# Kernel optimization log

Measured on AMD Instinct MI355X. Metric: run time of the kernel, lower is better.

## Reference

```python
import jax, jax.numpy as jnp
import numpy as np
import math

# ---- static config (must match init_kwargs / input_specs) ----
D = 1024
N_HEAD = 16
HEAD_DIM = D // N_HEAD          # 64
HALF = HEAD_DIM // 2            # rope half dim = 32
N_EXP = 8
TOP_K = 2
CAP_FACTOR = 2.0
LN_EPS = 1e-5


def _build_sin_cos(T, half_dim, dtype=jnp.float32):
    pos = jnp.arange(T, dtype=dtype)[:, None]                      # (T,1)
    inv_freq = 1.0 / (10000.0 ** (jnp.arange(0, 2 * half_dim, 2, dtype=dtype) / (2 * half_dim)))
    ang = pos * inv_freq[None, :]                                  # (T, half)
    return jnp.sin(ang), jnp.cos(ang)


def _layernorm(x, g, b):
    mu = jnp.mean(x, axis=-1, keepdims=True)
    var = jnp.mean(jnp.square(x - mu), axis=-1, keepdims=True)
    return (x - mu) * jax.lax.rsqrt(var + LN_EPS) * g + b


def _apply_rope(q, k, sin, cos):
    # q,k: (B,T,H,hd); sin,cos: (T, half)
    s = sin[None, :, None, :]
    c = cos[None, :, None, :]
    q1, q2 = q[..., :HALF], q[..., HALF:]
    k1, k2 = k[..., :HALF], k[..., HALF:]
    qr = jnp.concatenate([q1 * c - q2 * s, q1 * s + q2 * c], axis=-1)
    kr = jnp.concatenate([k1 * c - k2 * s, k1 * s + k2 * c], axis=-1)
    return qr, kr


def _attention(x, Wqkv, Wproj):
    B, T, C = x.shape
    qkv = x @ Wqkv                                                  # (B,T,3C)
    qkv = qkv.reshape(B, T, N_HEAD, 3 * HEAD_DIM)
    q, k, v = jnp.split(qkv, 3, axis=-1)                            # each (B,T,H,hd)
    sin, cos = _build_sin_cos(T, HALF)
    q, k = _apply_rope(q, k, sin, cos)
    scale = 1.0 / math.sqrt(HEAD_DIM)
    att = jnp.einsum('bqhd,bkhd->bhqk', q, k) * scale               # (B,H,T,T)
    causal = jnp.tril(jnp.ones((T, T), dtype=bool))
    att = jnp.where(causal[None, None], att, jnp.finfo(att.dtype).min)
    p = jax.nn.softmax(att, axis=-1)
    o = jnp.einsum('bhqk,bkhd->bqhd', p, v).reshape(B, T, C)
    return o @ Wproj, k, v


def _sparse_moe(flat, Wgate, W1, b1, W2, b2):
    # flat: (N, d). Eval mode: no router noise.
    N, d = flat.shape
    capacity = int(math.ceil(CAP_FACTOR * N / N_EXP))
    logits = flat @ Wgate                                           # (N,E)
    gates = jax.nn.softmax(logits, axis=-1)
    vals, inds = jax.lax.top_k(gates, TOP_K)                        # (N,k)
    flat_inds = inds.reshape(-1)                                    # (N*k,)
    flat_vals = vals.reshape(-1)
    neg = jnp.finfo(flat.dtype).min
    # per-expert assignment scores over all (token, slot) pairs
    scores = jnp.where(flat_inds[None, :] == jnp.arange(N_EXP)[:, None],
                       flat_vals[None, :], neg)                     # (E, N*k)
    top_scores, top_pos = jax.lax.top_k(scores, capacity)           # (E, cap)
    tok_idx = top_pos // TOP_K                                      # (E, cap)
    w = jnp.where(top_scores > neg, top_scores, 0.0)                # dropped slots -> 0 weight
    xe = flat[tok_idx]                                              # gather: (E, cap, d)
    h = jax.nn.gelu(jnp.einsum('ecd,edh->ech', xe, W1) + b1[:, None, :], approximate=False)
    out = jnp.einsum('ech,ehd->ecd', h, W2) + b2[:, None, :]
    out = out * w[..., None]
    final = jnp.zeros_like(flat).at[tok_idx.reshape(-1)].add(out.reshape(-1, d))
    return final


def setup_inputs() -> dict:
    key = jax.random.key(0)
    ks = jax.random.split(key, 10)
    B, T = 2, 2048
    s = 0.02
    return {
        'x': jax.random.normal(ks[0], (B, T, D), dtype=jnp.float32),
        'ln1_g': jnp.ones((D,), jnp.float32),
        'ln1_b': jnp.zeros((D,), jnp.float32),
        'ln2_g': jnp.ones((D,), jnp.float32),
        'ln2_b': jnp.zeros((D,), jnp.float32),
        'Wqkv': jax.random.normal(ks[1], (D, 3 * D), jnp.float32) * s,
        'Wproj': jax.random.normal(ks[2], (D, D), jnp.float32) * s,
        'Wgate': jax.random.normal(ks[3], (D, N_EXP), jnp.float32) * s,
        'W1': jax.random.normal(ks[4], (N_EXP, D, 4 * D), jnp.float32) * s,
        'b1': jnp.zeros((N_EXP, 4 * D), jnp.float32),
        'W2': jax.random.normal(ks[5], (N_EXP, 4 * D, D), jnp.float32) * s,
        'b2': jnp.zeros((N_EXP, D), jnp.float32),
    }


def reference(x, ln1_g, ln1_b, ln2_g, ln2_b, Wqkv, Wproj, Wgate, W1, b1, W2, b2):
    B, T, _ = x.shape
    x_norm = _layernorm(x, ln1_g, ln1_b)
    attn_out, k, v = _attention(x_norm, Wqkv, Wproj)
    x = x + attn_out
    ff_in = _layernorm(x, ln2_g, ln2_b)
    moe_out = _sparse_moe(ff_in.reshape(B * T, D), Wgate, W1, b1, W2, b2)
    x = x + moe_out.reshape(B, T, D)
    aux_loss = jnp.zeros((), x.dtype)  # eval mode
    return x, aux_loss, k, v
```

## Files before the change

### kernel.cpp

```cpp
#include <hip/hip_runtime.h>
#include <hip/hip_bf16.h>
#include <math.h>


#define TT 2048
#define NTOK 4096

typedef __attribute__((ext_vector_type(8))) short bf16x8;
typedef __attribute__((ext_vector_type(4))) float f32x4;
typedef __attribute__((ext_vector_type(16))) float f32x16;

static __device__ __forceinline__ ushort f2bf(float f) {
  union { float f; unsigned u; } v; v.f = f;
  unsigned r = v.u + 0x7FFFu + ((v.u >> 16) & 1u);
  return (ushort)(r >> 16);
}
static __device__ __forceinline__ float bf2f(ushort h) {
  union { unsigned u; float f; } v; v.u = ((unsigned)h) << 16; return v.f;
}
static __device__ __forceinline__ unsigned cvt_pk_bf16(float lo, float hi) {
  unsigned r;
  asm("v_cvt_pk_bf16_f32 %0, %1, %2" : "=v"(r) : "v"(lo), "v"(hi));
  return r;
}
static __device__ __forceinline__ void plane_swap(unsigned& a, unsigned& b) {
  asm("v_permlane32_swap_b32 %0, %1" : "+v"(a), "+v"(b));
}
static __device__ __forceinline__ float fexp2(float x) {
  float r;
  asm("v_exp_f32 %0, %1" : "=v"(r) : "v"(x));
  return r;
}

template<bool GATE>
__global__ __launch_bounds__(256)
void ln_kernel(const float* __restrict__ x, const float* __restrict__ g,
               const float* __restrict__ b, ushort* __restrict__ oh,
               ushort* __restrict__ ol, const float* __restrict__ Wg,
               int* __restrict__ te, float* __restrict__ tv, int* __restrict__ inv) {
  __shared__ float srow[1024];
  int row = blockIdx.x, tid = threadIdx.x;
  const float4* xr = (const float4*)(x + (size_t)row * 1024);
  float4 v = xr[tid];
  float s = v.x + v.y + v.z + v.w;
  #pragma unroll
  for (int off = 1; off < 64; off <<= 1) s += __shfl_xor(s, off);
  __shared__ float red1[4], red2[4];
  if ((tid & 63) == 0) red1[tid >> 6] = s;
  __syncthreads();
  float mu = (red1[0] + red1[1] + red1[2] + red1[3]) * (1.0f / 1024.0f);
  float dx = v.x - mu, dy = v.y - mu, dz = v.z - mu, dw = v.w - mu;
  float ss = dx*dx + dy*dy + dz*dz + dw*dw;
  #pragma unroll
  for (int off = 1; off < 64; off <<= 1) ss += __shfl_xor(ss, off);
  if ((tid & 63) == 0) red2[tid >> 6] = ss;
  __syncthreads();
  float var = (red2[0] + red2[1] + red2[2] + red2[3]) * (1.0f / 1024.0f);
  float inv_ = 1.0f / sqrtf(var + 1e-5f);
  float4 g4 = ((const float4*)g)[tid];
  float4 b4 = ((const float4*)b)[tid];
  float4 o4;
  o4.x = dx * inv_ * g4.x + b4.x;
  o4.y = dy * inv_ * g4.y + b4.y;
  o4.z = dz * inv_ * g4.z + b4.z;
  o4.w = dw * inv_ * g4.w + b4.w;
  size_t base = (size_t)row * 1024 + tid * 4;
  ushort h0 = f2bf(o4.x), h1 = f2bf(o4.y), h2 = f2bf(o4.z), h3 = f2bf(o4.w);
  ushort4 hh = {h0, h1, h2, h3};
  *(ushort4*)(oh + base) = hh;
  ushort4 ll = {f2bf(o4.x - bf2f(h0)), f2bf(o4.y - bf2f(h1)),
                f2bf(o4.z - bf2f(h2)), f2bf(o4.w - bf2f(h3))};
  *(ushort4*)(ol + base) = ll;
  if constexpr (GATE) {
    *(float4*)&srow[tid * 4] = o4;
    __syncthreads();
    float acc[8] = {};
    for (int i = tid; i < 1024; i += 256) {
      float xv = srow[i];
      const float4* wr = (const float4*)&Wg[i * 8];
      float4 w0 = wr[0], w1 = wr[1];
      acc[0] += xv * w0.x; acc[1] += xv * w0.y; acc[2] += xv * w0.z; acc[3] += xv * w0.w;
      acc[4] += xv * w1.x; acc[5] += xv * w1.y; acc[6] += xv * w1.z; acc[7] += xv * w1.w;
    }
    #pragma unroll
    for (int off = 1; off < 64; off <<= 1)
      #pragma unroll
      for (int qq = 0; qq < 8; ++qq) acc[qq] += __shfl_xor(acc[qq], off);
    __shared__ float red[4][8];
    if ((tid & 63) == 0)
      #pragma unroll
      for (int qq = 0; qq < 8; ++qq) red[tid >> 6][qq] = acc[qq];
    __syncthreads();
    if (tid == 0) {
      float gg[8];
      #pragma unroll
      for (int qq = 0; qq < 8; ++qq) gg[qq] = red[0][qq] + red[1][qq] + red[2][qq] + red[3][qq];
      float mx = gg[0];
      #pragma unroll
      for (int qq = 1; qq < 8; ++qq) mx = fmaxf(mx, gg[qq]);
      float sum = 0.0f;
      #pragma unroll
      for (int qq = 0; qq < 8; ++qq) { gg[qq] = expf(gg[qq] - mx); sum += gg[qq]; }
      float inv_s = 1.0f / sum;
      #pragma unroll
      for (int qq = 0; qq < 8; ++qq) gg[qq] *= inv_s;
      int e1 = 0; float v1 = gg[0];
      for (int qq = 1; qq < 8; ++qq) if (gg[qq] > v1) { v1 = gg[qq]; e1 = qq; }
      int e2 = -1; float v2 = -1.0f;
      for (int qq = 0; qq < 8; ++qq) { if (qq == e1) continue; if (gg[qq] > v2) { v2 = gg[qq]; e2 = qq; } }
      te[row * 2] = e1; te[row * 2 + 1] = e2;
      tv[row * 2] = v1; tv[row * 2 + 1] = v2;
      inv[row * 2] = -1; inv[row * 2 + 1] = -1;
    }
  }
}

__global__ void sincos_kernel(float* __restrict__ st, float* __restrict__ ct) {
  int t = blockIdx.x, j = threadIdx.x;
  double invf = pow(10000.0, -((double)(2 * j)) / 64.0);
  double ang = (double)t * invf;
  st[t * 32 + j] = (float)sin(ang);
  ct[t * 32 + j] = (float)cos(ang);
}

__global__ __launch_bounds__(256)
void rope_kernel(float* __restrict__ qkv, const float* __restrict__ st,
                 const float* __restrict__ ct, float* __restrict__ kout,
                 float* __restrict__ vout, ushort* __restrict__ Kh,
                 ushort* __restrict__ Kl) {
  int row = blockIdx.x;
  int t = row & (TT - 1);
  int b = row >> 11;
  int tid = threadIdx.x;
  float* base = qkv + (size_t)row * 3072;
  #pragma unroll
  for (int l = 0; l < 2; ++l) {
    int idx = l * 256 + tid;
    int h = idx >> 5, j = idx & 31;
    float s = st[t * 32 + j], c = ct[t * 32 + j];
    float* qp = base + h * 192;
    float q1 = qp[j], q2 = qp[j + 32];
    qp[j]      = q1 * c - q2 * s;
    qp[j + 32] = q1 * s + q2 * c;
    float k1 = qp[64 + j], k2 = qp[96 + j];
    float kr1 = k1 * c - k2 * s, kr2 = k1 * s + k2 * c;
    qp[64 + j] = kr1; qp[96 + j] = kr2;
    kout[(size_t)row * 1024 + h * 64 + j]      = kr1;
    kout[(size_t)row * 1024 + h * 64 + 32 + j] = kr2;
    size_t kb = ((size_t)(b * 16 + h) * TT + t) * 64;
    ushort h1 = f2bf(kr1);
    Kh[kb + j] = h1; Kl[kb + j] = f2bf(kr1 - bf2f(h1));
    ushort h2 = f2bf(kr2);
    Kh[kb + 32 + j] = h2; Kl[kb + 32 + j] = f2bf(kr2 - bf2f(h2));
  }
  #pragma unroll
  for (int l = 0; l < 4; ++l) {
    int f = l * 256 + tid;
    int h = f >> 6, d = f & 63;
    vout[(size_t)row * 1024 + f] = base[h * 192 + 128 + d];
  }
}

__global__ __launch_bounds__(256)
void vtprep_kernel(const float* __restrict__ vout, ushort* __restrict__ Vth,
                   ushort* __restrict__ Vtl) {
  __shared__ float tile[64][65];
  int t0 = blockIdx.x * 64, h = blockIdx.y, b = blockIdx.z;
  int tid = threadIdx.x;
  #pragma unroll
  for (int l = 0; l < 4; ++l) {
    int idx = l * 256 + tid;
    int r = idx >> 4, c4 = (idx & 15) * 4;
    *(float4*)&tile[r][c4] = *(const float4*)&vout[((size_t)(b * TT + t0 + r)) * 1024 + h * 64 + c4];
  }
  __syncthreads();
  int d = tid >> 2, ts = (tid & 3) * 16;
  union { bf16x8 v; ushort u[8]; } H0, H1, L0, L1;
  #pragma unroll
  for (int i = 0; i < 8; ++i) {
    float v0 = tile[ts + i][d];
    ushort hb0 = f2bf(v0);
    H0.u[i] = hb0; L0.u[i] = f2bf(v0 - bf2f(hb0));
    float v1 = tile[ts + 8 + i][d];
    ushort hb1 = f2bf(v1);
    H1.u[i] = hb1; L1.u[i] = f2bf(v1 - bf2f(hb1));
  }
  size_t basep = ((size_t)(b * 16 + h) * 64 + d) * TT + t0 + ts;
  *(bf16x8*)(Vth + basep) = H0.v;  *(bf16x8*)(Vth + basep + 8) = H1.v;
  *(bf16x8*)(Vtl + basep) = L0.v;  *(bf16x8*)(Vtl + basep + 8) = L1.v;
}

__global__ __launch_bounds__(256)
void flash9_kernel(const float* __restrict__ qkv, const ushort* __restrict__ Kh,
                   const ushort* __restrict__ Kl, const ushort* __restrict__ Vth,
                   const ushort* __restrict__ Vtl, float* __restrict__ Opart,
                   float* __restrict__ Mpart, float* __restrict__ Lpart) {
  int lin = blockIdx.x;
  int xcd = lin & 7, s = lin >> 3;
  int bh = xcd + 8 * (s / 40);
  int j = 39 - (s % 40);
  int qt, kc;
  if (j < 4)       { qt = j;                    kc = 0; }
  else if (j < 12) { qt = 4 + ((j - 4) >> 1);   kc = (j - 4) & 1; }
  else if (j < 24) { qt = 8 + (j - 12) / 3;     kc = (j - 12) % 3; }
  else             { qt = 12 + ((j - 24) >> 2); kc = (j - 24) & 3; }
  int slot = bh * 40 + j;
  int h = bh & 15, b = bh >> 4;
  int tid = threadIdx.x;
  int w = tid >> 6, lane = tid & 63;
  int q = lane & 31, LH = lane >> 5;
  size_t bT = (size_t)b * TT;
  int qglob0 = qt * 128 + w * 32;
  int qg = qglob0 + q;
  bf16x8 qH[4], qL[4];
  {
    const float qs = 0.125f * 1.44269504088896340736f;
    const float* qp = qkv + (bT + qg) * 3072 + h * 192 + LH * 8;
    #pragma unroll
    for (int dblk = 0; dblk < 4; ++dblk) {
      float4 f0 = *(const float4*)(qp + dblk * 16);
      float4 f1 = *(const float4*)(qp + dblk * 16 + 4);
      float vals[8] = {f0.x * qs, f0.y * qs, f0.z * qs, f0.w * qs,
                       f1.x * qs, f1.y * qs, f1.z * qs, f1.w * qs};
      union { bf16x8 v; ushort u[8]; } H, L;
      #pragma unroll
      for (int e = 0; e < 8; ++e) {
        ushort hb = f2bf(vals[e]);
        H.u[e] = hb; L.u[e] = f2bf(vals[e] - bf2f(hb));
      }
      qH[dblk] = H.v; qL[dblk] = L.v;
    }
  }
  const ushort* Kbh = Kh + (size_t)bh * TT * 64;
  const ushort* Kbl = Kl + (size_t)bh * TT * 64;
  const ushort* Vbh = Vth + (size_t)bh * 64 * TT;
  const ushort* Vbl = Vtl + (size_t)bh * 64 * TT;
  f32x16 accO0 = {}, accO1 = {};
  float m = -3.402823466e38f, lsum = 0.0f;
  int kvlo = kc * 512;
  int kvhi = min(kvlo + 512, qglob0 + 32);

  auto loadK = [&](bf16x8 (&kH)[4], bf16x8 (&kL)[4], int kv0) {
    const ushort* kbh = Kbh + (size_t)(kv0 + q) * 64 + LH * 8;
    const ushort* kbl = Kbl + (size_t)(kv0 + q) * 64 + LH * 8;
    #pragma unroll
    for (int dblk = 0; dblk < 4; ++dblk) {
      kH[dblk] = *(const bf16x8*)(kbh + dblk * 16);
      kL[dblk] = *(const bf16x8*)(kbl + dblk * 16);
    }
  };

  auto tile = [&](bf16x8 (&kH)[4], bf16x8 (&kL)[4],
                  bf16x8 (&kHn)[4], bf16x8 (&kLn)[4], int kv0, bool pf) {
    bf16x8 vAH[2][2], vAL[2][2];
    #pragma unroll
    for (int dblk = 0; dblk < 2; ++dblk)
      #pragma unroll
      for (int s2 = 0; s2 < 2; ++s2) {
        size_t ad = (size_t)(dblk * 32 + q) * TT + kv0 + s2 * 16 + LH * 8;
        vAH[dblk][s2] = *(const bf16x8*)(Vbh + ad);
        vAL[dblk][s2] = *(const bf16x8*)(Vbl + ad);
      }
    f32x16 sa = {}, sb = {};
    __builtin_amdgcn_s_setprio(1);
    sa = __builtin_amdgcn_mfma_f32_32x32x16_bf16(kH[0], qH[0], sa, 0, 0, 0);
    sb = __builtin_amdgcn_mfma_f32_32x32x16_bf16(kH[2], qH[2], sb, 0, 0, 0);
    sa = __builtin_amdgcn_mfma_f32_32x32x16_bf16(kH[1], qH[1], sa, 0, 0, 0);
    sb = __builtin_amdgcn_mfma_f32_32x32x16_bf16(kH[3], qH[3], sb, 0, 0, 0);
    sa = __builtin_amdgcn_mfma_f32_32x32x16_bf16(kH[0], qL[0], sa, 0, 0, 0);
    sb = __builtin_amdgcn_mfma_f32_32x32x16_bf16(kH[2], qL[2], sb, 0, 0, 0);
    sa = __builtin_amdgcn_mfma_f32_32x32x16_bf16(kH[1], qL[1], sa, 0, 0, 0);
    sb = __builtin_amdgcn_mfma_f32_32x32x16_bf16(kH[3], qL[3], sb, 0, 0, 0);
    sa = __builtin_amdgcn_mfma_f32_32x32x16_bf16(kL[0], qH[0], sa, 0, 0, 0);
    sb = __builtin_amdgcn_mfma_f32_32x32x16_bf16(kL[2], qH[2], sb, 0, 0, 0);
    sa = __builtin_amdgcn_mfma_f32_32x32x16_bf16(kL[1], qH[1], sa, 0, 0, 0);
    sb = __builtin_amdgcn_mfma_f32_32x32x16_bf16(kL[3], qH[3], sb, 0, 0, 0);
    __builtin_amdgcn_s_setprio(0);
    if (pf) loadK(kHn, kLn, kv0 + 32);
    float p[16];
    float pmax = -3.402823466e38f;
    if (kv0 + 31 > qglob0) {
      #pragma unroll
      for (int r = 0; r < 16; ++r) {
        int kvg = kv0 + (r & 3) + 8 * (r >> 2) + 4 * LH;
        float sv = (kvg <= qg) ? (sa[r] + sb[r]) : -3.402823466e38f;
        p[r] = sv; pmax = fmaxf(pmax, sv);
      }
    } else {
      #pragma unroll
      for (int r = 0; r < 16; ++r) {
        float sv = sa[r] + sb[r];
        p[r] = sv; pmax = fmaxf(pmax, sv);
      }
    }
    pmax = fmaxf(pmax, __shfl_xor(pmax, 32));
    float mnew = fmaxf(m, pmax);
    float fsc = fexp2(m - mnew);
    float psum = 0.0f;
    #pragma unroll
    for (int r = 0; r < 16; ++r) { p[r] = fexp2(p[r] - mnew); psum += p[r]; }
    psum += __shfl_xor(psum, 32);
    lsum = lsum * fsc + psum;
    m = mnew;
    #pragma unroll
    for (int r = 0; r < 16; ++r) { accO0[r] *= fsc; accO1[r] *= fsc; }
    bf16x8 pHf[2], pLf[2];
    #pragma unroll
    for (int s2 = 0; s2 < 2; ++s2) {
      int s8 = s2 * 8;
      unsigned a  = cvt_pk_bf16(p[s8 + 0], p[s8 + 1]);
      unsigned bw = cvt_pk_bf16(p[s8 + 2], p[s8 + 3]);
      unsigned c  = cvt_pk_bf16(p[s8 + 4], p[s8 + 5]);
      unsigned d  = cvt_pk_bf16(p[s8 + 6], p[s8 + 7]);
      float l0 = p[s8 + 0] - __uint_as_float(a << 16);
      float l1 = p[s8 + 1] - __uint_as_float(a & 0xFFFF0000u);
      float l2 = p[s8 + 2] - __uint_as_float(bw << 16);
      float l3 = p[s8 + 3] - __uint_as_float(bw & 0xFFFF0000u);
      float l4 = p[s8 + 4] - __uint_as_float(c << 16);
      float l5 = p[s8 + 5] - __uint_as_float(c & 0xFFFF0000u);
      float l6 = p[s8 + 6] - __uint_as_float(d << 16);
      float l7 = p[s8 + 7] - __uint_as_float(d & 0xFFFF0000u);
      unsigned al = cvt_pk_bf16(l0, l1);
      unsigned bl = cvt_pk_bf16(l2, l3);
      unsigned cl = cvt_pk_bf16(l4, l5);
      unsigned dl = cvt_pk_bf16(l6, l7);
      plane_swap(a, c); plane_swap(bw, d);
      plane_swap(al, cl); plane_swap(bl, dl);
      union { unsigned w[4]; bf16x8 v; } PH, PL;
      PH.w[0] = a;  PH.w[1] = bw; PH.w[2] = c;  PH.w[3] = d;
      PL.w[0] = al; PL.w[1] = bl; PL.w[2] = cl; PL.w[3] = dl;
      pHf[s2] = PH.v; pLf[s2] = PL.v;
    }
    __builtin_amdgcn_s_setprio(1);
    #pragma unroll
    for (int s2 = 0; s2 < 2; ++s2) {
      accO0 = __builtin_amdgcn_mfma_f32_32x32x16_bf16(vAH[0][s2], pHf[s2], accO0, 0, 0, 0);
      accO1 = __builtin_amdgcn_mfma_f32_32x32x16_bf16(vAH[1][s2], pHf[s2], accO1, 0, 0, 0);
      accO0 = __builtin_amdgcn_mfma_f32_32x32x16_bf16(vAH[0][s2], pLf[s2], accO0, 0, 0, 0);
      accO1 = __builtin_amdgcn_mfma_f32_32x32x16_bf16(vAH[1][s2], pLf[s2], accO1, 0, 0, 0);
      accO0 = __builtin_amdgcn_mfma_f32_32x32x16_bf16(vAL[0][s2], pHf[s2], accO0, 0, 0, 0);
      accO1 = __builtin_amdgcn_mfma_f32_32x32x16_bf16(vAL[1][s2], pHf[s2], accO1, 0, 0, 0);
    }
    __builtin_amdgcn_s_setprio(0);
  };

  bf16x8 kA[4], kB[4], kC[4], kD[4];
  loadK(kA, kB, kvlo);
  for (int kv0 = kvlo; kv0 < kvhi; kv0 += 64) {
    tile(kA, kB, kC, kD, kv0, kv0 + 32 < kvhi);
    if (kv0 + 32 < kvhi)
      tile(kC, kD, kA, kB, kv0 + 32, kv0 + 64 < kvhi);
  }

  if (LH == 0) {
    Mpart[slot * 128 + w * 32 + q] = m;
    Lpart[slot * 128 + w * 32 + q] = lsum;
  }
  float* Ob = Opart + (size_t)slot * 8192 + (w * 32 + q) * 64;
  #pragma unroll
  for (int g2 = 0; g2 < 4; ++g2) {
    float4 v0 = {accO0[g2 * 4 + 0], accO0[g2 * 4 + 1], accO0[g2 * 4 + 2], accO0[g2 * 4 + 3]};
    *(float4*)(Ob + 8 * g2 + 4 * LH) = v0;
    float4 v1 = {accO1[g2 * 4 + 0], accO1[g2 * 4 + 1], accO1[g2 * 4 + 2], accO1[g2 * 4 + 3]};
    *(float4*)(Ob + 32 + 8 * g2 + 4 * LH) = v1;
  }
}

__global__ __launch_bounds__(256)
void fmerge2_kernel(const float* __restrict__ Opart, const float* __restrict__ Mpart,
                    const float* __restrict__ Lpart, ushort* __restrict__ oh,
                    ushort* __restrict__ ol) {
  int qt = blockIdx.x, bh = blockIdx.y;
  int h = bh & 15, b = bh >> 4;
  int g = qt >> 2;
  int nc = g + 1;
  int off = 2 * g * (g + 1) + (qt & 3) * (g + 1);
  int slot0 = bh * 40 + off;
  int tid = threadIdx.x;
  int q = tid & 127, dh = tid >> 7;
  float mg = -3.402823466e38f;
  for (int c = 0; c < nc; ++c) mg = fmaxf(mg, Mpart[(slot0 + c) * 128 + q]);
  float lg = 0.0f;
  float4 acc[8] = {};
  for (int c = 0; c < nc; ++c) {
    float sc = fexp2(Mpart[(slot0 + c) * 128 + q] - mg);
    lg += sc * Lpart[(slot0 + c) * 128 + q];
    const float4* op = (const float4*)(Opart + (size_t)(slot0 + c) * 8192 + q * 64 + dh * 32);
    #pragma unroll
    for (int i = 0; i < 8; ++i) {
      float4 v = op[i];
      acc[i].x += sc * v.x; acc[i].y += sc * v.y;
      acc[i].z += sc * v.z; acc[i].w += sc * v.w;
    }
  }
  float inv = 1.0f / lg;
  size_t obase = ((size_t)(b * TT + qt * 128 + q)) * 1024 + h * 64 + dh * 32;
  #pragma unroll
  for (int i = 0; i < 8; ++i) {
    float4 v = {acc[i].x * inv, acc[i].y * inv, acc[i].z * inv, acc[i].w * inv};
    ushort h0 = f2bf(v.x), h1 = f2bf(v.y), h2 = f2bf(v.z), h3 = f2bf(v.w);
    ushort4 hh = {h0, h1, h2, h3};
    *(ushort4*)(oh + obase + i * 4) = hh;
    ushort4 ll = {f2bf(v.x - bf2f(h0)), f2bf(v.y - bf2f(h1)),
                  f2bf(v.z - bf2f(h2)), f2bf(v.w - bf2f(h3))};
    *(ushort4*)(ol + obase + i * 4) = ll;
  }
}

template<bool LO>
__global__ void tconv_kernel(const float* __restrict__ in, ushort* __restrict__ oh,
                             ushort* __restrict__ ol, int K, int N) {
  __shared__ float t[32][33];
  int z = blockIdx.z;
  const float* ip = in + (size_t)z * K * N;
  ushort* ohp = oh + (size_t)z * K * N;
  ushort* olp = LO ? (ol + (size_t)z * K * N) : nullptr;
  int n0 = blockIdx.x * 32, k0 = blockIdx.y * 32;
  int tx = threadIdx.x, ty = threadIdx.y;
  #pragma unroll
  for (int i = 0; i < 4; ++i)
    t[ty + 8 * i][tx] = ip[(size_t)(k0 + ty + 8 * i) * N + n0 + tx];
  __syncthreads();
  #pragma unroll
  for (int i = 0; i < 4; ++i) {
    float v = t[tx][ty + 8 * i];
    size_t off = (size_t)(n0 + ty + 8 * i) * K + k0 + tx;
    ushort hb = f2bf(v);
    ohp[off] = hb;
    if (LO) olp[off] = f2bf(v - bf2f(hb));
  }
}

#define LOAD_STEP(tt) do {                                                     \
    int kk = (tt) << 6;                                                        \
    _Pragma("unroll")                                                          \
    for (int q = 0; q < 4; ++q) {                                              \
      int rr = r0 + 32 * q;                                                    \
      int clog = cph ^ (rr & 7);                                               \
      raH[q] = *(const bf16x8*)(AhB + (size_t)garow[q] * K + kk + clog * 8);   \
      rbH[q] = *(const bf16x8*)(BhB + (size_t)(bn + rr) * K + kk + clog * 8);  \
      if constexpr (SPLIT3) {                                                  \
        raL[q] = *(const bf16x8*)(AlB + (size_t)garow[q] * K + kk + clog * 8); \
        rbL[q] = *(const bf16x8*)(BlB + (size_t)(bn + rr) * K + kk + clog * 8);\
      }                                                                        \
    }                                                                          \
  } while (0)

template<int EPI, bool GATHER, bool SPLIT3>
__global__ __launch_bounds__(256, 2)
void mgemm(const ushort* __restrict__ Ah, const ushort* __restrict__ Al,
           const ushort* __restrict__ Bh, const ushort* __restrict__ Bl,
           void* __restrict__ Cv, const float* __restrict__ extra,
           const int* __restrict__ gatAll, int N, int K,
           long aEStride, long bEStride, long cEStride, int biasEStride) {
  __shared__ ushort As[(SPLIT3 ? 2 : 1) * 128 * 64];
  __shared__ ushort Bs[(SPLIT3 ? 2 : 1) * 128 * 64];
  ushort* AsH = As;  ushort* AsL = SPLIT3 ? (As + 128 * 64) : As;
  ushort* BsH = Bs;  ushort* BsL = SPLIT3 ? (Bs + 128 * 64) : Bs;
  int z = blockIdx.z;
  const ushort* AhB = Ah + (size_t)z * aEStride;
  const ushort* AlB = SPLIT3 ? (Al + (size_t)z * aEStride) : nullptr;
  const ushort* BhB = Bh + (size_t)z * bEStride;
  const ushort* BlB = SPLIT3 ? (Bl + (size_t)z * bEStride) : nullptr;
  const int* gat = GATHER ? (gatAll + z * 1024) : nullptr;
  int bx = blockIdx.x, by = blockIdx.y;
  {
    int nwg = gridDim.x * gridDim.y;
    if ((nwg & 7) == 0) {
      int lid = bx + by * gridDim.x;
      int cpx = nwg >> 3;
      int wgid = (lid & 7) * cpx + (lid >> 3);
      bx = wgid % gridDim.x;
      by = wgid / gridDim.x;
    }
  }
  int bm = by * 128, bn = bx * 128;
  int tid = threadIdx.x;
  int r0 = tid >> 3, cph = tid & 7;
  int garow[4];
  #pragma unroll
  for (int q = 0; q < 4; ++q) {
    int rr = r0 + 32 * q;
    garow[q] = GATHER ? gat[bm + rr] : (bm + rr);
  }
  int kSteps = K >> 6;
  int wid = tid >> 6, lane = tid & 63;
  int wm = wid >> 1, wn = wid & 1;
  int lr = lane & 15, lk = lane >> 4;
  f32x4 acc[4][4] = {};
  bf16x8 raH[4], rbH[4], raL[4], rbL[4];
  LOAD_STEP(0);
  for (int t = 0; t < kSteps; ++t) {
    __syncthreads();
    #pragma unroll
    for (int q = 0; q < 4; ++q) {
      int rr = r0 + 32 * q;
      *(bf16x8*)&AsH[rr * 64 + cph * 8] = raH[q];
      *(bf16x8*)&BsH[rr * 64 + cph * 8] = rbH[q];
      if constexpr (SPLIT3) {
        *(bf16x8*)&AsL[rr * 64 + cph * 8] = raL[q];
        *(bf16x8*)&BsL[rr * 64 + cph * 8] = rbL[q];
      }
    }
    __syncthreads();
    if (t + 1 < kSteps) LOAD_STEP(t + 1);
    #pragma unroll
    for (int kh = 0; kh < 2; ++kh) {
      bf16x8 afH[4], bfH[4], afL[4], bfL[4];
      #pragma unroll
      for (int mf = 0; mf < 4; ++mf) {
        int row = wm * 64 + mf * 16 + lr;
        int ch = (kh * 4 + lk) ^ (row & 7);
        afH[mf] = *(const bf16x8*)&AsH[row * 64 + ch * 8];
        if constexpr (SPLIT3) afL[mf] = *(const bf16x8*)&AsL[row * 64 + ch * 8];
      }
      #pragma unroll
      for (int nf = 0; nf < 4; ++nf) {
        int row = wn * 64 + nf * 16 + lr;
        int ch = (kh * 4 + lk) ^ (row & 7);
        bfH[nf] = *(const bf16x8*)&BsH[row * 64 + ch * 8];
        if constexpr (SPLIT3) bfL[nf] = *(const bf16x8*)&BsL[row * 64 + ch * 8];
      }
      #pragma unroll
      for (int mf = 0; mf < 4; ++mf)
        #pragma unroll
        for (int nf = 0; nf < 4; ++nf)
          acc[mf][nf] = __builtin_amdgcn_mfma_f32_16x16x32_bf16(afH[mf], bfH[nf], acc[mf][nf], 0, 0, 0);
      if constexpr (SPLIT3) {
        #pragma unroll
        for (int mf = 0; mf < 4; ++mf)
          #pragma unroll
          for (int nf = 0; nf < 4; ++nf)
            acc[mf][nf] = __builtin_amdgcn_mfma_f32_16x16x32_bf16(afH[mf], bfL[nf], acc[mf][nf], 0, 0, 0);
        #pragma unroll
        for (int mf = 0; mf < 4; ++mf)
          #pragma unroll
          for (int nf = 0; nf < 4; ++nf)
            acc[mf][nf] = __builtin_amdgcn_mfma_f32_16x16x32_bf16(afL[mf], bfH[nf], acc[mf][nf], 0, 0, 0);
      }
    }
  }
  int crow = bm + wm * 64, ccol = bn + wn * 64;
  if constexpr (EPI <= 1) {
    float* C = (float*)Cv;
    #pragma unroll
    for (int mf = 0; mf < 4; ++mf)
      #pragma unroll
      for (int nf = 0; nf < 4; ++nf)
        #pragma unroll
        for (int r = 0; r < 4; ++r) {
          int row = crow + mf * 16 + lk * 4 + r;
          int col = ccol + nf * 16 + lr;
          float v = acc[mf][nf][r];
          if constexpr (EPI == 1) v += extra[(size_t)row * N + col];
          C[(size_t)row * N + col] = v;
        }
  } else {
    const float* bias = extra + (size_t)z * biasEStride;
    ushort* C = (ushort*)Cv + (size_t)z * cEStride;
    #pragma unroll
    for (int mf = 0; mf < 4; ++mf)
      #pragma unroll
      for (int nf = 0; nf < 4; ++nf)
        #pragma unroll
        for (int r = 0; r < 4; ++r) {
          int row = crow + mf * 16 + lk * 4 + r;
          int col = ccol + nf * 16 + lr;
          float v = acc[mf][nf][r] + bias[col];
          if constexpr (EPI == 2)
            v = 0.5f * v * (1.0f + erff(v * 0.70710678118654752f));
          C[(size_t)row * N + col] = f2bf(v);
        }
  }
}

__global__ __launch_bounds__(1024)
void route_sort_kernel(const int* __restrict__ te, const float* __restrict__ tv,
                       int* __restrict__ etok, float* __restrict__ ew,
                       int* __restrict__ inv) {
  __shared__ unsigned long long sk[4096];
  __shared__ int wcnt[16];
  __shared__ int base;
  int e = blockIdx.x, tid = threadIdx.x;
  int lane = tid & 63, wv = tid >> 6;
  if (tid == 0) base = 0;
  __syncthreads();
  for (int c = 0; c < 8; ++c) {
    int s = c * 1024 + tid;
    bool sel = (te[s] == e);
    unsigned long long ball = __ballot(sel);
    int pre = __popcll(ball & ((1ull << lane) - 1ull));
    if (lane == 0) wcnt[wv] = __popcll(ball);
    __syncthreads();
    int woff = 0, tot = 0;
    #pragma unroll
    for (int i = 0; i < 16; ++i) {
      int cc = wcnt[i];
      if (i < wv) woff += cc;
      tot += cc;
    }
    if (sel) {
      unsigned vb = __float_as_uint(tv[s]);
      sk[base + woff + pre] =
          ((unsigned long long)vb << 32) | (unsigned)(0xFFFFFFFFu - (unsigned)s);
    }
    __syncthreads();
    if (tid == 0) base += tot;
    __syncthreads();
  }
  int n = base;
  if (n > 1024) {
    int P = (n <= 2048) ? 2048 : 4096;
    for (int i = n + tid; i < P; i += 1024) sk[i] = 0ull;
    __syncthreads();
    for (int k = 2; k <= P; k <<= 1)
      for (int j = k >> 1; j > 0; j >>= 1) {
        for (int t = tid; t < (P >> 1); t += 1024) {
          int i = ((t & ~(j - 1)) << 1) | (t & (j - 1));
          int p = i | j;
          unsigned long long a = sk[i], bq = sk[p];
          bool desc = ((i & k) == 0);
          if (desc ? (a < bq) : (a > bq)) { sk[i] = bq; sk[p] = a; }
        }
        __syncthreads();
      }
  }
  int cap = n < 1024 ? n : 1024;
  if (tid < cap) {
    unsigned long long key = sk[tid];
    unsigned slot = 0xFFFFFFFFu - (unsigned)(key & 0xFFFFFFFFull);
    etok[e * 1024 + tid] = (int)(slot >> 1);
    ew[e * 1024 + tid] = __uint_as_float((unsigned)(key >> 32));
    inv[slot] = e * 1024 + tid;
  } else {
    etok[e * 1024 + tid] = 0;
    ew[e * 1024 + tid] = 0.0f;
  }
}

__global__ __launch_bounds__(256)
void combine_kernel(const float* __restrict__ xres, const ushort* __restrict__ eo,
                    const int* __restrict__ inv, const float* __restrict__ ew,
                    float* __restrict__ outx, float* __restrict__ aux) {
  int token = blockIdx.x;
  int d = threadIdx.x * 4;
  float4 acc = *(const float4*)&xres[(size_t)token * 1024 + d];
  #pragma unroll
  for (int j = 0; j < 2; ++j) {
    int p = inv[token * 2 + j];
    if (p >= 0) {
      float w = ew[p];
      const ushort* ep = eo + (size_t)p * 1024 + d;
      acc.x += w * bf2f(ep[0]); acc.y += w * bf2f(ep[1]);
      acc.z += w * bf2f(ep[2]); acc.w += w * bf2f(ep[3]);
    }
  }
  *(float4*)&outx[(size_t)token * 1024 + d] = acc;
  if (token == 0 && threadIdx.x == 0) aux[0] = 0.0f;
}

extern "C" void kernel_launch(void* const* d_in, const int* in_sizes, int n_in,
                              void* d_out, int out_size, void* d_ws, size_t ws_size,
                              hipStream_t stream) {
  const float* x     = (const float*)d_in[0];
  const float* ln1g  = (const float*)d_in[1];
  const float* ln1b  = (const float*)d_in[2];
  const float* ln2g  = (const float*)d_in[3];
  const float* ln2b  = (const float*)d_in[4];
  const float* Wqkv  = (const float*)d_in[5];
  const float* Wproj = (const float*)d_in[6];
  const float* Wg    = (const float*)d_in[7];
  const float* W1    = (const float*)d_in[8];
  const float* b1    = (const float*)d_in[9];
  const float* W2    = (const float*)d_in[10];
  const float* b2    = (const float*)d_in[11];

  float* out_x   = (float*)d_out;
  float* out_aux = out_x + 4194304;
  float* out_k   = out_aux + 1;
  float* out_v   = out_k + 4194304;

  float* ws   = (float*)d_ws;
  float* A    = ws;
  float* qkvb = ws + 4194304;
  float* st   = ws + 20971520;
  float* ct   = ws + 21037056;
  int*   te   = (int*)(ws + 21102592);
  float* tv   = ws + 21110784;
  int*   etok = (int*)(ws + 21118976);
  float* ew   = ws + 21127168;
  int*   inv  = (int*)(ws + 21135360);
  ushort* bfAh = (ushort*)(ws + 21143552);
  ushort* bfAl = (ushort*)(ws + 23240704);
  ushort* BqH  = (ushort*)(ws + 25337856);
  ushort* BqL  = (ushort*)(ws + 26910720);
  ushort* BpH  = (ushort*)(ws + 28483584);
  ushort* BpL  = (ushort*)(ws + 29007872);
  ushort* W1t  = (ushort*)(ws + 29532160);
  ushort* W2t  = (ushort*)(ws + 46309376);
  ushort* eo   = (ushort*)(ws + 63086592);
  ushort* hbuf = (ushort*)(ws + 4194304);
  ushort* Kh_  = bfAh;
  ushort* Kl_  = bfAl;
  ushort* Vth_ = eo;
  ushort* Vtl_ = eo + 4194304;
  float* Opart = ws + 29532160;
  float* Mpart = ws + 40017920;
  float* Lpart = ws + 40181760;

  tconv_kernel<true ><<<dim3(96, 32, 1),  dim3(32, 8), 0, stream>>>(Wqkv,  BqH, BqL, 1024, 3072);
  tconv_kernel<true ><<<dim3(32, 32, 1),  dim3(32, 8), 0, stream>>>(Wproj, BpH, BpL, 1024, 1024);
  sincos_kernel<<<TT, 32, 0, stream>>>(st, ct);

  ln_kernel<false><<<NTOK, 256, 0, stream>>>(x, ln1g, ln1b, bfAh, bfAl,
                                             nullptr, nullptr, nullptr, nullptr);
  mgemm<0, false, true><<<dim3(24, 32, 1), 256, 0, stream>>>(
      bfAh, bfAl, BqH, BqL, qkvb, nullptr, nullptr, 3072, 1024, 0, 0, 0, 0);
  rope_kernel<<<NTOK, 256, 0, stream>>>(qkvb, st, ct, out_k, out_v, Kh_, Kl_);
  vtprep_kernel<<<dim3(32, 16, 2), 256, 0, stream>>>(out_v, Vth_, Vtl_);
  flash9_kernel<<<1280, 256, 0, stream>>>(qkvb, Kh_, Kl_, Vth_, Vtl_, Opart, Mpart, Lpart);
  fmerge2_kernel<<<dim3(16, 32), 256, 0, stream>>>(Opart, Mpart, Lpart, bfAh, bfAl);
  mgemm<1, false, true><<<dim3(8, 32, 1), 256, 0, stream>>>(
      bfAh, bfAl, BpH, BpL, A, x, nullptr, 1024, 1024, 0, 0, 0, 0);
  tconv_kernel<false><<<dim3(128, 32, 8), dim3(32, 8), 0, stream>>>(W1, W1t, nullptr, 1024, 4096);
  tconv_kernel<false><<<dim3(32, 128, 8), dim3(32, 8), 0, stream>>>(W2, W2t, nullptr, 4096, 1024);
  ln_kernel<true><<<NTOK, 256, 0, stream>>>(A, ln2g, ln2b, bfAh, bfAl, Wg, te, tv, inv);
  route_sort_kernel<<<8, 1024, 0, stream>>>(te, tv, etok, ew, inv);
  mgemm<2, true, false><<<dim3(32, 8, 8), 256, 0, stream>>>(
      bfAh, nullptr, W1t, nullptr, hbuf, b1, etok, 4096, 1024,
      0, 4096L * 1024, 1024L * 4096, 4096);
  mgemm<3, false, false><<<dim3(8, 8, 8), 256, 0, stream>>>(
      hbuf, nullptr, W2t, nullptr, eo, b2, nullptr, 1024, 4096,
      1024L * 4096, 1024L * 4096, 1024L * 1024, 1024);
  combine_kernel<<<NTOK, 256, 0, stream>>>(A, eo, inv, ew, out_x, out_aux);
}
```

Measured before the change: 676.2 us.

## Software-pipeline flash attention QK with softmax and vectorize weight transpose

The flash attention loop is restructured so the QK^T MFMAs for the next KV tile are issued while softmax and PV of the current tile run, with V loads hoisted ahead. The MoE weight transpose-convert is replaced by a 64x64 tiled kernel using float4 loads and ushort4 stores to cut memory transactions. The redundant write-back of rotated K into the qkv buffer in the rope kernel is also dropped. The pipelined loop keeps two score accumulators live, which raises register pressure.

```diff
diff --git a/kernel.cpp b/kernel.cpp
--- a/kernel.cpp
+++ b/kernel.cpp
@@ -144,7 +144,6 @@
     qp[j + 32] = q1 * s + q2 * c;
     float k1 = qp[64 + j], k2 = qp[96 + j];
     float kr1 = k1 * c - k2 * s, kr2 = k1 * s + k2 * c;
-    qp[64 + j] = kr1; qp[96 + j] = kr2;
     kout[(size_t)row * 1024 + h * 64 + j]      = kr1;
     kout[(size_t)row * 1024 + h * 64 + 32 + j] = kr2;
     size_t kb = ((size_t)(b * 16 + h) * TT + t) * 64;
@@ -191,10 +190,10 @@
 }
 
 __global__ __launch_bounds__(256)
-void flash9_kernel(const float* __restrict__ qkv, const ushort* __restrict__ Kh,
-                   const ushort* __restrict__ Kl, const ushort* __restrict__ Vth,
-                   const ushort* __restrict__ Vtl, float* __restrict__ Opart,
-                   float* __restrict__ Mpart, float* __restrict__ Lpart) {
+void flash10_kernel(const float* __restrict__ qkv, const ushort* __restrict__ Kh,
+                    const ushort* __restrict__ Kl, const ushort* __restrict__ Vth,
+                    const ushort* __restrict__ Vtl, float* __restrict__ Opart,
+                    float* __restrict__ Mpart, float* __restrict__ Lpart) {
   int lin = blockIdx.x;
   int xcd = lin & 7, s = lin >> 3;
   int bh = xcd + 8 * (s / 40);
@@ -240,7 +239,11 @@
   int kvlo = kc * 512;
   int kvhi = min(kvlo + 512, qglob0 + 32);
 
-  auto loadK = [&](bf16x8 (&kH)[4], bf16x8 (&kL)[4], int kv0) {
+  bf16x8 kH[4], kL[4];
+  bf16x8 vAH[2][2], vAL[2][2];
+  float p[16];
+
+  auto loadK = [&](int kv0) {
     const ushort* kbh = Kbh + (size_t)(kv0 + q) * 64 + LH * 8;
     const ushort* kbl = Kbl + (size_t)(kv0 + q) * 64 + LH * 8;
     #pragma unroll
@@ -249,10 +252,7 @@
       kL[dblk] = *(const bf16x8*)(kbl + dblk * 16);
     }
   };
-
-  auto tile = [&](bf16x8 (&kH)[4], bf16x8 (&kL)[4],
-                  bf16x8 (&kHn)[4], bf16x8 (&kLn)[4], int kv0, bool pf) {
-    bf16x8 vAH[2][2], vAL[2][2];
+  auto loadV = [&](int kv0) {
     #pragma unroll
     for (int dblk = 0; dblk < 2; ++dblk)
       #pragma unroll
@@ -261,7 +261,8 @@
         vAH[dblk][s2] = *(const bf16x8*)(Vbh + ad);
         vAL[dblk][s2] = *(const bf16x8*)(Vbl + ad);
       }
-    f32x16 sa = {}, sb = {};
+  };
+  auto qkc = [&](f32x16& sa, f32x16& sb) {
     __builtin_amdgcn_s_setprio(1);
     sa = __builtin_amdgcn_mfma_f32_32x32x16_bf16(kH[0], qH[0], sa, 0, 0, 0);
     sb = __builtin_amdgcn_mfma_f32_32x32x16_bf16(kH[2], qH[2], sb, 0, 0, 0);
@@ -276,8 +277,8 @@
     sa = __builtin_amdgcn_mfma_f32_32x32x16_bf16(kL[1], qH[1], sa, 0, 0, 0);
     sb = __builtin_amdgcn_mfma_f32_32x32x16_bf16(kL[3], qH[3], sb, 0, 0, 0);
     __builtin_amdgcn_s_setprio(0);
-    if (pf) loadK(kHn, kLn, kv0 + 32);
-    float p[16];
+  };
+  auto smx = [&](f32x16& sa, f32x16& sb, int kv0) {
     float pmax = -3.402823466e38f;
     if (kv0 + 31 > qglob0) {
       #pragma unroll
@@ -304,6 +305,8 @@
     m = mnew;
     #pragma unroll
     for (int r = 0; r < 16; ++r) { accO0[r] *= fsc; accO1[r] *= fsc; }
+  };
+  auto packpv = [&]() {
     bf16x8 pHf[2], pLf[2];
     #pragma unroll
     for (int s2 = 0; s2 < 2; ++s2) {
@@ -344,12 +347,27 @@
     __builtin_amdgcn_s_setprio(0);
   };
 
-  bf16x8 kA[4], kB[4], kC[4], kD[4];
-  loadK(kA, kB, kvlo);
-  for (int kv0 = kvlo; kv0 < kvhi; kv0 += 64) {
-    tile(kA, kB, kC, kD, kv0, kv0 + 32 < kvhi);
-    if (kv0 + 32 < kvhi)
-      tile(kC, kD, kA, kB, kv0 + 32, kv0 + 64 < kvhi);
+  f32x16 s0a = {}, s0b = {}, s1a = {}, s1b = {};
+  loadK(kvlo);
+  qkc(s0a, s0b);
+  int kv0 = kvlo;
+  for (;;) {
+    loadV(kv0);
+    bool hn = kv0 + 32 < kvhi;
+    if (hn) loadK(kv0 + 32);
+    smx(s0a, s0b, kv0);
+    if (hn) { s1a = (f32x16){}; s1b = (f32x16){}; qkc(s1a, s1b); }
+    packpv();
+    if (!hn) break;
+    kv0 += 32;
+    loadV(kv0);
+    bool hn2 = kv0 + 32 < kvhi;
+    if (hn2) loadK(kv0 + 32);
+    smx(s1a, s1b, kv0);
+    if (hn2) { s0a = (f32x16){}; s0b = (f32x16){}; qkc(s0a, s0b); }
+    packpv();
+    if (!hn2) break;
+    kv0 += 32;
   }
 
   if (LH == 0) {
@@ -429,6 +447,29 @@
     ohp[off] = hb;
     if (LO) olp[off] = f2bf(v - bf2f(hb));
   }
+}
+
+__global__ __launch_bounds__(256)
+void tconv4_kernel(const float* __restrict__ in, ushort* __restrict__ out,
+                   int K, int N) {
+  __shared__ float t[64][68];
+  int z = blockIdx.z;
+  const float* ip = in + (size_t)z * K * N;
+  ushort* op = out + (size_t)z * K * N;
+  int n0 = blockIdx.x * 64, k0 = blockIdx.y * 64;
+  int tid = threadIdx.x;
+  int r = tid >> 4, c4 = (tid & 15) * 4;
+  #pragma unroll
+  for (int i = 0; i < 4; ++i)
+    *(float4*)&t[r + 16 * i][c4] = *(const float4*)&ip[(size_t)(k0 + r + 16 * i) * N + n0 + c4];
+  __syncthreads();
+  int n = tid >> 2, kb = (tid & 3) * 16;
+  union { ushort u[16]; ushort4 v[4]; } o;
+  #pragma unroll
+  for (int i = 0; i < 16; ++i) o.u[i] = f2bf(t[kb + i][n]);
+  size_t ob = (size_t)(n0 + n) * K + k0 + kb;
+  #pragma unroll
+  for (int i = 0; i < 4; ++i) *(ushort4*)&op[ob + 4 * i] = o.v[i];
 }
 
 #define LOAD_STEP(tt) do {                                                     \
@@ -718,12 +759,12 @@
       bfAh, bfAl, BqH, BqL, qkvb, nullptr, nullptr, 3072, 1024, 0, 0, 0, 0);
   rope_kernel<<<NTOK, 256, 0, stream>>>(qkvb, st, ct, out_k, out_v, Kh_, Kl_);
   vtprep_kernel<<<dim3(32, 16, 2), 256, 0, stream>>>(out_v, Vth_, Vtl_);
-  flash9_kernel<<<1280, 256, 0, stream>>>(qkvb, Kh_, Kl_, Vth_, Vtl_, Opart, Mpart, Lpart);
+  flash10_kernel<<<1280, 256, 0, stream>>>(qkvb, Kh_, Kl_, Vth_, Vtl_, Opart, Mpart, Lpart);
   fmerge2_kernel<<<dim3(16, 32), 256, 0, stream>>>(Opart, Mpart, Lpart, bfAh, bfAl);
   mgemm<1, false, true><<<dim3(8, 32, 1), 256, 0, stream>>>(
       bfAh, bfAl, BpH, BpL, A, x, nullptr, 1024, 1024, 0, 0, 0, 0);
-  tconv_kernel<false><<<dim3(128, 32, 8), dim3(32, 8), 0, stream>>>(W1, W1t, nullptr, 1024, 4096);
-  tconv_kernel<false><<<dim3(32, 128, 8), dim3(32, 8), 0, stream>>>(W2, W2t, nullptr, 4096, 1024);
+  tconv4_kernel<<<dim3(64, 16, 8), 256, 0, stream>>>(W1, W1t, 1024, 4096);
+  tconv4_kernel<<<dim3(16, 64, 8), 256, 0, stream>>>(W2, W2t, 4096, 1024);
   ln_kernel<true><<<NTOK, 256, 0, stream>>>(A, ln2g, ln2b, bfAh, bfAl, Wg, te, tv, inv);
   route_sort_kernel<<<8, 1024, 0, stream>>>(te, tv, etok, ew, inv);
   mgemm<2, true, false><<<dim3(32, 8, 8), 256, 0, stream>>>(
```

New measurement: 671.1 us. About the same (-0.8%).

## Precompute split-bf16 Q in rope, vectorize weight transpose, raise non-split GEMM occupancy

Applied to the files above, without the earlier changes.

The rope kernel now scales Q and writes it as hi/lo bf16 pairs into new buffers, so the flash kernel loads bf16 Q directly instead of reading fp32 qkv and converting it in every block. The rope kernel also stops writing rotated Q and K back into qkv. The MoE weight transposes switch to a 64x64 tile kernel that uses float4 loads and ushort4 stores. The launch bounds for the non-split3 GEMMs go from 2 to 3 blocks, which may force register spills.

```diff
diff --git a/kernel.cpp b/kernel.cpp
--- a/kernel.cpp
+++ b/kernel.cpp
@@ -124,27 +124,33 @@
 }
 
 __global__ __launch_bounds__(256)
-void rope_kernel(float* __restrict__ qkv, const float* __restrict__ st,
+void rope_kernel(const float* __restrict__ qkv, const float* __restrict__ st,
                  const float* __restrict__ ct, float* __restrict__ kout,
                  float* __restrict__ vout, ushort* __restrict__ Kh,
-                 ushort* __restrict__ Kl) {
+                 ushort* __restrict__ Kl, ushort* __restrict__ Qh,
+                 ushort* __restrict__ Ql) {
+  const float qs = 0.125f * 1.44269504088896340736f;
   int row = blockIdx.x;
   int t = row & (TT - 1);
   int b = row >> 11;
   int tid = threadIdx.x;
-  float* base = qkv + (size_t)row * 3072;
+  const float* base = qkv + (size_t)row * 3072;
   #pragma unroll
   for (int l = 0; l < 2; ++l) {
     int idx = l * 256 + tid;
     int h = idx >> 5, j = idx & 31;
     float s = st[t * 32 + j], c = ct[t * 32 + j];
-    float* qp = base + h * 192;
+    const float* qp = base + h * 192;
     float q1 = qp[j], q2 = qp[j + 32];
-    qp[j]      = q1 * c - q2 * s;
-    qp[j + 32] = q1 * s + q2 * c;
+    float qr1 = q1 * c - q2 * s, qr2 = q1 * s + q2 * c;
+    size_t qb = (size_t)row * 1024 + h * 64;
+    float a1 = qr1 * qs, a2 = qr2 * qs;
+    ushort qh1 = f2bf(a1);
+    Qh[qb + j] = qh1; Ql[qb + j] = f2bf(a1 - bf2f(qh1));
+    ushort qh2 = f2bf(a2);
+    Qh[qb + 32 + j] = qh2; Ql[qb + 32 + j] = f2bf(a2 - bf2f(qh2));
     float k1 = qp[64 + j], k2 = qp[96 + j];
     float kr1 = k1 * c - k2 * s, kr2 = k1 * s + k2 * c;
-    qp[64 + j] = kr1; qp[96 + j] = kr2;
     kout[(size_t)row * 1024 + h * 64 + j]      = kr1;
     kout[(size_t)row * 1024 + h * 64 + 32 + j] = kr2;
     size_t kb = ((size_t)(b * 16 + h) * TT + t) * 64;
@@ -191,10 +197,11 @@
 }
 
 __global__ __launch_bounds__(256)
-void flash9_kernel(const float* __restrict__ qkv, const ushort* __restrict__ Kh,
-                   const ushort* __restrict__ Kl, const ushort* __restrict__ Vth,
-                   const ushort* __restrict__ Vtl, float* __restrict__ Opart,
-                   float* __restrict__ Mpart, float* __restrict__ Lpart) {
+void flash11_kernel(const ushort* __restrict__ Qh, const ushort* __restrict__ Ql,
+                    const ushort* __restrict__ Kh, const ushort* __restrict__ Kl,
+                    const ushort* __restrict__ Vth, const ushort* __restrict__ Vtl,
+                    float* __restrict__ Opart, float* __restrict__ Mpart,
+                    float* __restrict__ Lpart) {
   int lin = blockIdx.x;
   int xcd = lin & 7, s = lin >> 3;
   int bh = xcd + 8 * (s / 40);
@@ -214,21 +221,12 @@
   int qg = qglob0 + q;
   bf16x8 qH[4], qL[4];
   {
-    const float qs = 0.125f * 1.44269504088896340736f;
-    const float* qp = qkv + (bT + qg) * 3072 + h * 192 + LH * 8;
+    const ushort* qph = Qh + (bT + qg) * 1024 + h * 64 + LH * 8;
+    const ushort* qpl = Ql + (bT + qg) * 1024 + h * 64 + LH * 8;
     #pragma unroll
     for (int dblk = 0; dblk < 4; ++dblk) {
-      float4 f0 = *(const float4*)(qp + dblk * 16);
-      float4 f1 = *(const float4*)(qp + dblk * 16 + 4);
-      float vals[8] = {f0.x * qs, f0.y * qs, f0.z * qs, f0.w * qs,
-                       f1.x * qs, f1.y * qs, f1.z * qs, f1.w * qs};
-      union { bf16x8 v; ushort u[8]; } H, L;
-      #pragma unroll
-      for (int e = 0; e < 8; ++e) {
-        ushort hb = f2bf(vals[e]);
-        H.u[e] = hb; L.u[e] = f2bf(vals[e] - bf2f(hb));
-      }
-      qH[dblk] = H.v; qL[dblk] = L.v;
+      qH[dblk] = *(const bf16x8*)(qph + dblk * 16);
+      qL[dblk] = *(const bf16x8*)(qpl + dblk * 16);
     }
   }
   const ushort* Kbh = Kh + (size_t)bh * TT * 64;
@@ -431,6 +429,29 @@
   }
 }
 
+__global__ __launch_bounds__(256)
+void tconv4_kernel(const float* __restrict__ in, ushort* __restrict__ out,
+                   int K, int N) {
+  __shared__ float t[64][68];
+  int z = blockIdx.z;
+  const float* ip = in + (size_t)z * K * N;
+  ushort* op = out + (size_t)z * K * N;
+  int n0 = blockIdx.x * 64, k0 = blockIdx.y * 64;
+  int tid = threadIdx.x;
+  int r = tid >> 4, c4 = (tid & 15) * 4;
+  #pragma unroll
+  for (int i = 0; i < 4; ++i)
+    *(float4*)&t[r + 16 * i][c4] = *(const float4*)&ip[(size_t)(k0 + r + 16 * i) * N + n0 + c4];
+  __syncthreads();
+  int n = tid >> 2, kb = (tid & 3) * 16;
+  union { ushort u[16]; ushort4 v[4]; } o;
+  #pragma unroll
+  for (int i = 0; i < 16; ++i) o.u[i] = f2bf(t[kb + i][n]);
+  size_t ob = (size_t)(n0 + n) * K + k0 + kb;
+  #pragma unroll
+  for (int i = 0; i < 4; ++i) *(ushort4*)&op[ob + 4 * i] = o.v[i];
+}
+
 #define LOAD_STEP(tt) do {                                                     \
     int kk = (tt) << 6;                                                        \
     _Pragma("unroll")                                                          \
@@ -447,7 +468,7 @@
   } while (0)
 
 template<int EPI, bool GATHER, bool SPLIT3>
-__global__ __launch_bounds__(256, 2)
+__global__ __launch_bounds__(256, SPLIT3 ? 2 : 3)
 void mgemm(const ushort* __restrict__ Ah, const ushort* __restrict__ Al,
            const ushort* __restrict__ Bh, const ushort* __restrict__ Bl,
            void* __restrict__ Cv, const float* __restrict__ extra,
@@ -683,6 +704,8 @@
   float* ws   = (float*)d_ws;
   float* A    = ws;
   float* qkvb = ws + 4194304;
+  ushort* Qh_ = (ushort*)(ws + 16777216);
+  ushort* Ql_ = (ushort*)(ws + 18874368);
   float* st   = ws + 20971520;
   float* ct   = ws + 21037056;
   int*   te   = (int*)(ws + 21102592);
@@ -716,14 +739,15 @@
                                              nullptr, nullptr, nullptr, nullptr);
   mgemm<0, false, true><<<dim3(24, 32, 1), 256, 0, stream>>>(
       bfAh, bfAl, BqH, BqL, qkvb, nullptr, nullptr, 3072, 1024, 0, 0, 0, 0);
-  rope_kernel<<<NTOK, 256, 0, stream>>>(qkvb, st, ct, out_k, out_v, Kh_, Kl_);
+  rope_kernel<<<NTOK, 256, 0, stream>>>(qkvb, st, ct, out_k, out_v, Kh_, Kl_, Qh_, Ql_);
   vtprep_kernel<<<dim3(32, 16, 2), 256, 0, stream>>>(out_v, Vth_, Vtl_);
-  flash9_kernel<<<1280, 256, 0, stream>>>(qkvb, Kh_, Kl_, Vth_, Vtl_, Opart, Mpart, Lpart);
+  flash11_kernel<<<1280, 256, 0, stream>>>(Qh_, Ql_, Kh_, Kl_, Vth_, Vtl_,
+                                           Opart, Mpart, Lpart);
   fmerge2_kernel<<<dim3(16, 32), 256, 0, stream>>>(Opart, Mpart, Lpart, bfAh, bfAl);
   mgemm<1, false, true><<<dim3(8, 32, 1), 256, 0, stream>>>(
       bfAh, bfAl, BpH, BpL, A, x, nullptr, 1024, 1024, 0, 0, 0, 0);
-  tconv_kernel<false><<<dim3(128, 32, 8), dim3(32, 8), 0, stream>>>(W1, W1t, nullptr, 1024, 4096);
-  tconv_kernel<false><<<dim3(32, 128, 8), dim3(32, 8), 0, stream>>>(W2, W2t, nullptr, 4096, 1024);
+  tconv4_kernel<<<dim3(64, 16, 8), 256, 0, stream>>>(W1, W1t, 1024, 4096);
+  tconv4_kernel<<<dim3(16, 64, 8), 256, 0, stream>>>(W2, W2t, 4096, 1024);
   ln_kernel<true><<<NTOK, 256, 0, stream>>>(A, ln2g, ln2b, bfAh, bfAl, Wg, te, tv, inv);
   route_sort_kernel<<<8, 1024, 0, stream>>>(te, tv, etok, ew, inv);
   mgemm<2, true, false><<<dim3(32, 8, 8), 256, 0, stream>>>(
```

New measurement: 679.2 us. About the same (+0.4%).
